# Performance work log

Hardware: AMD Instinct MI355X
Metric: run time of the kernel (lower is better)

Reference implementation:

```python
import jax, jax.numpy as jnp
import numpy as np

D_MODEL = 1024
NUM_HEADS = 16
HEAD_DIM = D_MODEL // NUM_HEADS


def setup_inputs() -> dict:
    key = jax.random.key(0)
    ks = jax.random.split(key, 9)
    B, S, D = 4, 2048, D_MODEL
    scale = 1.0 / np.sqrt(D)
    x = jax.random.normal(ks[0], (B, S, D), dtype=jnp.float32)
    wq = jax.random.normal(ks[1], (D, D), dtype=jnp.float32) * scale
    wk = jax.random.normal(ks[2], (D, D), dtype=jnp.float32) * scale
    wv = jax.random.normal(ks[3], (D, D), dtype=jnp.float32) * scale
    wo = jax.random.normal(ks[4], (D, D), dtype=jnp.float32) * scale
    bq = jax.random.normal(ks[5], (D,), dtype=jnp.float32) * 0.02
    bk = jax.random.normal(ks[6], (D,), dtype=jnp.float32) * 0.02
    bv = jax.random.normal(ks[7], (D,), dtype=jnp.float32) * 0.02
    bo = jax.random.normal(ks[8], (D,), dtype=jnp.float32) * 0.02
    return {"x": x, "wq": wq, "bq": bq, "wk": wk, "bk": bk,
            "wv": wv, "bv": bv, "wo": wo, "bo": bo}


def _split_heads(t):  # [B,S,D] -> [B,H,S,Dh]
    B, S, _ = t.shape
    return t.reshape(B, S, NUM_HEADS, HEAD_DIM).transpose(0, 2, 1, 3)


def reference(x, wq, bq, wk, bk, wv, bv, wo, bo):
    B, S, D = x.shape
    q = _split_heads(x @ wq + bq)  # [B,H,S,Dh]
    k = _split_heads(x @ wk + bk)
    v = _split_heads(x @ wv + bv)
    scores = jnp.einsum("bhqd,bhkd->bhqk", q, k) / jnp.sqrt(
        jnp.asarray(HEAD_DIM, dtype=x.dtype))
    causal = jnp.tril(jnp.ones((S, S), dtype=bool))  # [S,S]
    scores = jnp.where(causal, scores, jnp.finfo(scores.dtype).min)
    attn = jax.nn.softmax(scores, axis=-1)
    ctx = jnp.einsum("bhqk,bhkd->bhqd", attn, v)  # [B,H,S,Dh]
    ctx = ctx.transpose(0, 2, 1, 3).reshape(B, S, D)
    return ctx @ wo + bo
```

## Files before the change

### kernel.cpp

```cpp
#include <hip/hip_runtime.h>
#include <hip/hip_bf16.h>
#include <stdint.h>

#define DMODEL 1024
#define NH 16
#define DH 64
#define BATCH 4
#define SEQ 2048

#if __has_builtin(__builtin_amdgcn_exp2f)
#define EXP2F(x) __builtin_amdgcn_exp2f(x)
#else
#define EXP2F(x) exp2f(x)
#endif

typedef __attribute__((ext_vector_type(8))) short short8;
typedef __attribute__((ext_vector_type(4))) float f32x4;
typedef __attribute__((ext_vector_type(4))) ushort ushort4v;

__device__ __forceinline__ ushort f2bf(float f) {
    union { float f; unsigned u; } v; v.f = f;
    unsigned r = v.u + 0x7fffu + ((v.u >> 16) & 1u);
    return (ushort)(r >> 16);
}

__global__ __launch_bounds__(256) void convert_bf16(const float* __restrict__ src,
                                                    ushort* __restrict__ dst) {
    const size_t i = ((size_t)blockIdx.x * 256 + threadIdx.x) * 8;
    float4 a = *(const float4*)(src + i);
    float4 b = *(const float4*)(src + i + 4);
    short8 r;
    r[0] = (short)f2bf(a.x); r[1] = (short)f2bf(a.y);
    r[2] = (short)f2bf(a.z); r[3] = (short)f2bf(a.w);
    r[4] = (short)f2bf(b.x); r[5] = (short)f2bf(b.y);
    r[6] = (short)f2bf(b.z); r[7] = (short)f2bf(b.w);
    *(short8*)(dst + i) = r;
}

__global__ __launch_bounds__(256) void transpose_cvt_w4(
    const float* __restrict__ s0, const float* __restrict__ s1,
    const float* __restrict__ s2, const float* __restrict__ s3,
    ushort* __restrict__ d0, ushort* __restrict__ d1,
    ushort* __restrict__ d2, ushort* __restrict__ d3) {
    __shared__ ushort tile[64][65];
    const int z = blockIdx.z;
    const float* src = (z == 0) ? s0 : (z == 1) ? s1 : (z == 2) ? s2 : s3;
    ushort* dst = (z == 0) ? d0 : (z == 1) ? d1 : (z == 2) ? d2 : d3;
    const int bx = blockIdx.x * 64;
    const int by = blockIdx.y * 64;
    const int tx = threadIdx.x & 63, ty = threadIdx.x >> 6;
    #pragma unroll
    for (int i = 0; i < 64; i += 4)
        tile[ty + i][tx] = f2bf(src[(size_t)(by + ty + i) * DMODEL + bx + tx]);
    __syncthreads();
    #pragma unroll
    for (int i = 0; i < 64; i += 4)
        dst[(size_t)(bx + ty + i) * DMODEL + by + tx] = tile[tx][ty + i];
}

template <int MODE>
__global__ __launch_bounds__(256) void gemm_bt(
    const ushort* __restrict__ A, const ushort* __restrict__ Bt,
    const float* __restrict__ b0, const float* __restrict__ b1,
    const float* __restrict__ b2,
    void* __restrict__ o0v, void* __restrict__ o1v, void* __restrict__ o2v) {
    __shared__ __align__(16) ushort smem[8192];
    const int lane = threadIdx.x & 63;
    const int wv   = threadIdx.x >> 6;
    const int mBase = blockIdx.y * 128;
    const int nBase = blockIdx.x * 128;
    const int wm = (wv >> 1) * 64;
    const int wn = (wv & 1) * 64;

    f32x4 acc[4][4];
    #pragma unroll
    for (int i = 0; i < 4; ++i)
        #pragma unroll
        for (int j = 0; j < 4; ++j) acc[i][j] = (f32x4){0.f, 0.f, 0.f, 0.f};

    const int lrow = lane >> 2;
    const int lcol = (lane & 3) * 8;
    const int frow = lane & 15;
    const int fcol = (lane >> 4) * 8;

    for (int k0 = 0; k0 < DMODEL; k0 += 32) {
        #pragma unroll
        for (int i = 0; i < 2; ++i) {
            const int c = wv * 2 + i;
            const ushort* ga = A + (size_t)(mBase + c * 16 + lrow) * DMODEL + k0 + lcol;
            __builtin_amdgcn_global_load_lds(
                (const __attribute__((address_space(1))) void*)ga,
                (__attribute__((address_space(3))) void*)&smem[c * 512], 16, 0, 0);
            const ushort* gb = Bt + (size_t)(nBase + c * 16 + lrow) * DMODEL + k0 + lcol;
            __builtin_amdgcn_global_load_lds(
                (const __attribute__((address_space(1))) void*)gb,
                (__attribute__((address_space(3))) void*)&smem[4096 + c * 512], 16, 0, 0);
        }
        __syncthreads();
        short8 af[4], bfr[4];
        #pragma unroll
        for (int t = 0; t < 4; ++t)
            af[t] = *(const short8*)&smem[(wm + t * 16 + frow) * 32 + fcol];
        #pragma unroll
        for (int t = 0; t < 4; ++t)
            bfr[t] = *(const short8*)&smem[4096 + (wn + t * 16 + frow) * 32 + fcol];
        #pragma unroll
        for (int i = 0; i < 4; ++i)
            #pragma unroll
            for (int j = 0; j < 4; ++j)
                acc[i][j] = __builtin_amdgcn_mfma_f32_16x16x32_bf16(af[i], bfr[j],
                                                                   acc[i][j], 0, 0, 0);
        __syncthreads();
    }

    const int orow = (lane >> 4) * 4;
    const int ocol = lane & 15;

    if (MODE == 1) {
        #pragma unroll
        for (int i = 0; i < 4; ++i)
            #pragma unroll
            for (int j = 0; j < 4; ++j)
                #pragma unroll
                for (int r = 0; r < 4; ++r) {
                    const int m = mBase + wm + i * 16 + orow + r;
                    const int n = nBase + wn + j * 16 + ocol;
                    ((float*)o0v)[(size_t)m * DMODEL + n] = acc[i][j][r] + b0[n];
                }
        return;
    }

    ushort* sw = &smem[wv * 2048];
    const int mat = nBase >> 10;
    const int nb0 = (nBase & 1023) + wn;
    const int hb  = nb0 >> 6;
    const float* bp = (mat == 0) ? b0 : ((mat == 1) ? b1 : b2);
    float bj[4];
    #pragma unroll
    for (int j = 0; j < 4; ++j) bj[j] = bp[nb0 + j * 16 + ocol];
    const int bbq = (mBase + wm) >> 11;
    const int s0w = (mBase + wm) & 2047;
    const float qscale = (mat == 0) ? 0.1803368801f : 1.0f;

    if (mat < 2) {
        ushort* obase = (ushort*)((mat == 0) ? o0v : o1v) +
                        ((size_t)(bbq * NH + hb) * SEQ + s0w) * DH;
        const int row = lane >> 2, cc = lane & 3;
        #pragma unroll
        for (int i = 0; i < 4; ++i) {
            #pragma unroll
            for (int j = 0; j < 4; ++j)
                #pragma unroll
                for (int r = 0; r < 4; ++r)
                    sw[(orow + r) * 72 + j * 16 + ocol] =
                        f2bf((acc[i][j][r] + bj[j]) * qscale);
            asm volatile("s_waitcnt lgkmcnt(0)" ::: "memory");
            #pragma unroll
            for (int p = 0; p < 2; ++p) {
                short8 v8 = *(const short8*)&sw[row * 72 + cc * 8 + p * 32];
                *(short8*)&obase[(size_t)(i * 16 + row) * DH + cc * 8 + p * 32] = v8;
            }
            asm volatile("s_waitcnt lgkmcnt(0)" ::: "memory");
        }
    } else {
        ushort* op = (ushort*)o2v;
        const int rowd = lane >> 2, sc = lane & 3;
        #pragma unroll
        for (int j = 0; j < 4; ++j) {
            #pragma unroll
            for (int i = 0; i < 4; ++i)
                #pragma unroll
                for (int r = 0; r < 4; ++r)
                    sw[ocol * 72 + i * 16 + orow + r] = f2bf(acc[i][j][r] + bj[j]);
            asm volatile("s_waitcnt lgkmcnt(0)" ::: "memory");
            ushort* vbase = op + ((size_t)(bbq * NH + hb) * DH + j * 16 + rowd) * SEQ + s0w;
            #pragma unroll
            for (int p = 0; p < 2; ++p) {
                short8 v8 = *(const short8*)&sw[rowd * 72 + sc * 8 + p * 32];
                *(short8*)&vbase[sc * 8 + p * 32] = v8;
            }
            asm volatile("s_waitcnt lgkmcnt(0)" ::: "memory");
        }
    }
}

#define PSTR 72
__global__ __launch_bounds__(256, 4) void flash_attn(
    const ushort* __restrict__ Q, const ushort* __restrict__ K,
    const ushort* __restrict__ Vt, ushort* __restrict__ ctx) {
    __shared__ __align__(16) ushort Ks[4096];
    __shared__ __align__(16) ushort Vs[4096];
    __shared__ __align__(16) ushort plds[4][16 * PSTR];
    const int lane = threadIdx.x & 63;
    const int wv   = threadIdx.x >> 6;
    const int bh   = blockIdx.x & 63;
    const int Jp   = blockIdx.x >> 6;
    const int bb = bh >> 4, h = bh & 15;

    const ushort* Qb = Q + (size_t)bh * SEQ * DH;
    const ushort* Kb = K + (size_t)bh * SEQ * DH;
    const ushort* Vb = Vt + (size_t)bh * DH * SEQ;

    const int frow = lane & 15;
    const int fq   = lane >> 4;
    const int r7s  = lane >> 3;
    const int csw  = (lane & 7) ^ r7s;

    short8 ones;
    #pragma unroll
    for (int i = 0; i < 8; ++i) ones[i] = (short)0x3F80;

    #pragma unroll 1
    for (int half = 0; half < 2; ++half) {
        const int Je = half ? (31 - Jp) : Jp;
        const int q0 = Je * 64 + wv * 16;
        const int qmax = q0 + 15;

        short8 qf[2];
        #pragma unroll
        for (int ks = 0; ks < 2; ++ks)
            qf[ks] = *(const short8*)&Qb[(size_t)(q0 + frow) * DH + ks * 32 + fq * 8];

        f32x4 o[4], lacc;
        #pragma unroll
        for (int t = 0; t < 4; ++t) o[t] = (f32x4){0.f, 0.f, 0.f, 0.f};
        lacc = (f32x4){0.f, 0.f, 0.f, 0.f};

        #pragma unroll 1
        for (int it = 0; it <= Je; ++it) {
            const int k0 = it * 64;
            __syncthreads();
            #pragma unroll
            for (int i = 0; i < 2; ++i) {
                const int c = wv * 2 + i;
                const ushort* gk = Kb + (size_t)(k0 + c * 8 + r7s) * DH + csw * 8;
                __builtin_amdgcn_global_load_lds(
                    (const __attribute__((address_space(1))) void*)gk,
                    (__attribute__((address_space(3))) void*)&Ks[c * 512], 16, 0, 0);
                const ushort* gv = Vb + (size_t)(c * 8 + r7s) * SEQ + k0 + csw * 8;
                __builtin_amdgcn_global_load_lds(
                    (const __attribute__((address_space(1))) void*)gv,
                    (__attribute__((address_space(3))) void*)&Vs[c * 512], 16, 0, 0);
            }
            __syncthreads();

            if (it < Je) {
                f32x4 sacc[4];
                #pragma unroll
                for (int nt = 0; nt < 4; ++nt) sacc[nt] = (f32x4){0.f, 0.f, 0.f, 0.f};
                #pragma unroll
                for (int nt = 0; nt < 4; ++nt) {
                    const int row = nt * 16 + frow, r7 = row & 7;
                    #pragma unroll
                    for (int ks = 0; ks < 2; ++ks) {
                        short8 kf = *(const short8*)
                            &Ks[(row >> 3) * 512 + r7 * 64 + (((ks * 4 + fq) ^ r7) * 8)];
                        sacc[nt] = __builtin_amdgcn_mfma_f32_16x16x32_bf16(kf, qf[ks],
                                                                          sacc[nt], 0, 0, 0);
                    }
                }
                #pragma unroll
                for (int nt = 0; nt < 4; ++nt) {
                    float p0 = EXP2F(sacc[nt][0]);
                    float p1 = EXP2F(sacc[nt][1]);
                    float p2 = EXP2F(sacc[nt][2]);
                    float p3 = EXP2F(sacc[nt][3]);
                    uint2 dw;
                    dw.x = __builtin_amdgcn_perm(__float_as_uint(p1), __float_as_uint(p0),
                                                 0x07060302u);
                    dw.y = __builtin_amdgcn_perm(__float_as_uint(p3), __float_as_uint(p2),
                                                 0x07060302u);
                    *(uint2*)&plds[wv][frow * PSTR + nt * 16 + fq * 4] = dw;
                }
                asm volatile("s_waitcnt lgkmcnt(0)" ::: "memory");
                #pragma unroll
                for (int kc = 0; kc < 2; ++kc) {
                    short8 pf = *(const short8*)&plds[wv][frow * PSTR + kc * 32 + fq * 8];
                    lacc = __builtin_amdgcn_mfma_f32_16x16x32_bf16(ones, pf, lacc, 0, 0, 0);
                    #pragma unroll
                    for (int t = 0; t < 4; ++t) {
                        const int row = t * 16 + frow, r7 = row & 7;
                        short8 vf = *(const short8*)
                            &Vs[(row >> 3) * 512 + r7 * 64 + (((kc * 4 + fq) ^ r7) * 8)];
                        o[t] = __builtin_amdgcn_mfma_f32_16x16x32_bf16(vf, pf, o[t], 0, 0, 0);
                    }
                }
            } else {
                const int qrow = q0 + frow;
                f32x4 sacc[4];
                #pragma unroll
                for (int nt = 0; nt < 4; ++nt) sacc[nt] = (f32x4){0.f, 0.f, 0.f, 0.f};
                #pragma unroll
                for (int nt = 0; nt < 4; ++nt)
                    if (k0 + nt * 16 <= qmax) {
                        const int row = nt * 16 + frow, r7 = row & 7;
                        #pragma unroll
                        for (int ks = 0; ks < 2; ++ks) {
                            short8 kf = *(const short8*)
                                &Ks[(row >> 3) * 512 + r7 * 64 + (((ks * 4 + fq) ^ r7) * 8)];
                            sacc[nt] = __builtin_amdgcn_mfma_f32_16x16x32_bf16(kf, qf[ks],
                                                                              sacc[nt], 0, 0, 0);
                        }
                    }
                #pragma unroll
                for (int nt = 0; nt < 4; ++nt) {
                    uint2 dw; dw.x = 0u; dw.y = 0u;
                    if (k0 + nt * 16 <= qmax) {
                        float pp[4];
                        #pragma unroll
                        for (int r = 0; r < 4; ++r) {
                            const float e = EXP2F(sacc[nt][r]);
                            pp[r] = (k0 + nt * 16 + fq * 4 + r <= qrow) ? e : 0.f;
                        }
                        dw.x = __builtin_amdgcn_perm(__float_as_uint(pp[1]),
                                                     __float_as_uint(pp[0]), 0x07060302u);
                        dw.y = __builtin_amdgcn_perm(__float_as_uint(pp[3]),
                                                     __float_as_uint(pp[2]), 0x07060302u);
                    }
                    *(uint2*)&plds[wv][frow * PSTR + nt * 16 + fq * 4] = dw;
                }
                asm volatile("s_waitcnt lgkmcnt(0)" ::: "memory");
                #pragma unroll
                for (int kc = 0; kc < 2; ++kc) {
                    if (k0 + kc * 32 <= qmax) {
                        short8 pf = *(const short8*)&plds[wv][frow * PSTR + kc * 32 + fq * 8];
                        lacc = __builtin_amdgcn_mfma_f32_16x16x32_bf16(ones, pf, lacc, 0, 0, 0);
                        #pragma unroll
                        for (int t = 0; t < 4; ++t) {
                            const int row = t * 16 + frow, r7 = row & 7;
                            short8 vf = *(const short8*)
                                &Vs[(row >> 3) * 512 + r7 * 64 + (((kc * 4 + fq) ^ r7) * 8)];
                            o[t] = __builtin_amdgcn_mfma_f32_16x16x32_bf16(vf, pf, o[t], 0, 0, 0);
                        }
                    }
                }
            }
        }
        const float inv = 1.0f / lacc[0];
        const int qrow = q0 + frow;
        ushort* cp = ctx + (size_t)(bb * SEQ + qrow) * DMODEL + h * DH;
        #pragma unroll
        for (int t = 0; t < 4; ++t) {
            ushort4v ov;
            #pragma unroll
            for (int r = 0; r < 4; ++r) ov[r] = f2bf(o[t][r] * inv);
            *(ushort4v*)&cp[t * 16 + fq * 4] = ov;
        }
    }
}

extern "C" void kernel_launch(void* const* d_in, const int* in_sizes, int n_in,
                              void* d_out, int out_size, void* d_ws, size_t ws_size,
                              hipStream_t stream) {
    const float* x  = (const float*)d_in[0];
    const float* wq = (const float*)d_in[1];
    const float* bq = (const float*)d_in[2];
    const float* wk = (const float*)d_in[3];
    const float* bk = (const float*)d_in[4];
    const float* wvp = (const float*)d_in[5];
    const float* bv = (const float*)d_in[6];
    const float* wo = (const float*)d_in[7];
    const float* bo = (const float*)d_in[8];
    float* out = (float*)d_out;
    ushort* ws = (ushort*)d_ws;

    const size_t QSZ = (size_t)BATCH * NH * SEQ * DH;
    ushort* xbf   = ws;
    ushort* qws   = ws + QSZ;
    ushort* kws   = ws + 2 * QSZ;
    ushort* vtws  = ws + 3 * QSZ;
    ushort* ctxws = ws + 4 * QSZ;
    ushort* wtqkv = ws + 5 * QSZ;
    ushort* wto   = wtqkv + 3 * (size_t)DMODEL * DMODEL;

    dim3 tb(256);
    convert_bf16<<<dim3(4096), tb, 0, stream>>>(x, xbf);
    transpose_cvt_w4<<<dim3(16, 16, 4), tb, 0, stream>>>(
        wq, wk, wvp, wo,
        wtqkv, wtqkv + (size_t)DMODEL * DMODEL, wtqkv + 2 * (size_t)DMODEL * DMODEL, wto);

    gemm_bt<0><<<dim3(24, 64), tb, 0, stream>>>(xbf, wtqkv, bq, bk, bv,
                                                qws, kws, vtws);
    flash_attn<<<dim3(1024), tb, 0, stream>>>(qws, kws, vtws, ctxws);
    gemm_bt<1><<<dim3(8, 64), tb, 0, stream>>>(ctxws, wto, bo, nullptr, nullptr,
                                               out, nullptr, nullptr);
}
```

Measured before the change: 259.6 us.

## Double-buffer K/V in flash attention, fuse prep kernels, swizzle GEMM tiles per XCD

Flash attention now double-buffers the K and V tiles in LDS, issuing the next tile's global-to-LDS loads before computing the current one, with one barrier per iteration instead of two. This is meant to hide load latency. The diagonal and off-diagonal paths are merged into one loop body, and the P staging buffer is shrunk to half the width. The x conversion and weight transposes are fused into a single prep launch, and GEMM blocks are remapped so neighbouring M tiles land on the same XCD for L2 reuse. Doubling the K/V buffers raises LDS use per block, which could lower occupancy.

```diff
diff --git a/kernel.cpp b/kernel.cpp
--- a/kernel.cpp
+++ b/kernel.cpp
@@ -24,30 +24,38 @@
     return (ushort)(r >> 16);
 }
 
-__global__ __launch_bounds__(256) void convert_bf16(const float* __restrict__ src,
-                                                    ushort* __restrict__ dst) {
-    const size_t i = ((size_t)blockIdx.x * 256 + threadIdx.x) * 8;
-    float4 a = *(const float4*)(src + i);
-    float4 b = *(const float4*)(src + i + 4);
-    short8 r;
-    r[0] = (short)f2bf(a.x); r[1] = (short)f2bf(a.y);
-    r[2] = (short)f2bf(a.z); r[3] = (short)f2bf(a.w);
-    r[4] = (short)f2bf(b.x); r[5] = (short)f2bf(b.y);
-    r[6] = (short)f2bf(b.z); r[7] = (short)f2bf(b.w);
-    *(short8*)(dst + i) = r;
-}
-
-__global__ __launch_bounds__(256) void transpose_cvt_w4(
-    const float* __restrict__ s0, const float* __restrict__ s1,
-    const float* __restrict__ s2, const float* __restrict__ s3,
-    ushort* __restrict__ d0, ushort* __restrict__ d1,
-    ushort* __restrict__ d2, ushort* __restrict__ d3) {
+#define GLL(gp, lp) __builtin_amdgcn_global_load_lds( \
+    (const __attribute__((address_space(1))) void*)(gp), \
+    (__attribute__((address_space(3))) void*)(lp), 16, 0, 0)
+
+__global__ __launch_bounds__(256) void prep(
+    const float* __restrict__ x,
+    const float* __restrict__ wq, const float* __restrict__ wk,
+    const float* __restrict__ wv, const float* __restrict__ wo,
+    ushort* __restrict__ xbf,
+    ushort* __restrict__ dq, ushort* __restrict__ dk,
+    ushort* __restrict__ dv, ushort* __restrict__ dwo) {
+    const int z = blockIdx.z;
+    if (z == 4) {
+        size_t base = (size_t)(blockIdx.y * 16 + blockIdx.x) * 32768 +
+                      (size_t)threadIdx.x * 8;
+        #pragma unroll 1
+        for (int t = 0; t < 16; ++t, base += 2048) {
+            float4 a = *(const float4*)(x + base);
+            float4 c = *(const float4*)(x + base + 4);
+            short8 r;
+            r[0] = (short)f2bf(a.x); r[1] = (short)f2bf(a.y);
+            r[2] = (short)f2bf(a.z); r[3] = (short)f2bf(a.w);
+            r[4] = (short)f2bf(c.x); r[5] = (short)f2bf(c.y);
+            r[6] = (short)f2bf(c.z); r[7] = (short)f2bf(c.w);
+            *(short8*)(xbf + base) = r;
+        }
+        return;
+    }
     __shared__ ushort tile[64][65];
-    const int z = blockIdx.z;
-    const float* src = (z == 0) ? s0 : (z == 1) ? s1 : (z == 2) ? s2 : s3;
-    ushort* dst = (z == 0) ? d0 : (z == 1) ? d1 : (z == 2) ? d2 : d3;
-    const int bx = blockIdx.x * 64;
-    const int by = blockIdx.y * 64;
+    const float* src = (z == 0) ? wq : (z == 1) ? wk : (z == 2) ? wv : wo;
+    ushort* dst = (z == 0) ? dq : (z == 1) ? dk : (z == 2) ? dv : dwo;
+    const int bx = blockIdx.x * 64, by = blockIdx.y * 64;
     const int tx = threadIdx.x & 63, ty = threadIdx.x >> 6;
     #pragma unroll
     for (int i = 0; i < 64; i += 4)
@@ -67,8 +75,12 @@
     __shared__ __align__(16) ushort smem[8192];
     const int lane = threadIdx.x & 63;
     const int wv   = threadIdx.x >> 6;
-    const int mBase = blockIdx.y * 128;
-    const int nBase = blockIdx.x * 128;
+    constexpr int NTILES = (MODE == 0) ? 24 : 8;
+    const int L   = blockIdx.y * NTILES + blockIdx.x;
+    const int xcd = L & 7;
+    const int idx = L >> 3;
+    const int mBase = (xcd * 8 + idx / NTILES) * 128;
+    const int nBase = (idx % NTILES) * 128;
     const int wm = (wv >> 1) * 64;
     const int wn = (wv & 1) * 64;
 
@@ -87,14 +99,9 @@
         #pragma unroll
         for (int i = 0; i < 2; ++i) {
             const int c = wv * 2 + i;
-            const ushort* ga = A + (size_t)(mBase + c * 16 + lrow) * DMODEL + k0 + lcol;
-            __builtin_amdgcn_global_load_lds(
-                (const __attribute__((address_space(1))) void*)ga,
-                (__attribute__((address_space(3))) void*)&smem[c * 512], 16, 0, 0);
-            const ushort* gb = Bt + (size_t)(nBase + c * 16 + lrow) * DMODEL + k0 + lcol;
-            __builtin_amdgcn_global_load_lds(
-                (const __attribute__((address_space(1))) void*)gb,
-                (__attribute__((address_space(3))) void*)&smem[4096 + c * 512], 16, 0, 0);
+            GLL(A + (size_t)(mBase + c * 16 + lrow) * DMODEL + k0 + lcol, &smem[c * 512]);
+            GLL(Bt + (size_t)(nBase + c * 16 + lrow) * DMODEL + k0 + lcol,
+                &smem[4096 + c * 512]);
         }
         __syncthreads();
         short8 af[4], bfr[4];
@@ -184,13 +191,13 @@
     }
 }
 
-#define PSTR 72
+#define PSTR2 40
 __global__ __launch_bounds__(256, 4) void flash_attn(
     const ushort* __restrict__ Q, const ushort* __restrict__ K,
     const ushort* __restrict__ Vt, ushort* __restrict__ ctx) {
-    __shared__ __align__(16) ushort Ks[4096];
-    __shared__ __align__(16) ushort Vs[4096];
-    __shared__ __align__(16) ushort plds[4][16 * PSTR];
+    __shared__ __align__(16) ushort Ks[2][4096];
+    __shared__ __align__(16) ushort Vs[2][4096];
+    __shared__ __align__(16) ushort plds[4][16 * PSTR2];
     const int lane = threadIdx.x & 63;
     const int wv   = threadIdx.x >> 6;
     const int bh   = blockIdx.x & 63;
@@ -215,6 +222,7 @@
         const int Je = half ? (31 - Jp) : Jp;
         const int q0 = Je * 64 + wv * 16;
         const int qmax = q0 + 15;
+        const int qrow = q0 + frow;
 
         short8 qf[2];
         #pragma unroll
@@ -225,119 +233,88 @@
         #pragma unroll
         for (int t = 0; t < 4; ++t) o[t] = (f32x4){0.f, 0.f, 0.f, 0.f};
         lacc = (f32x4){0.f, 0.f, 0.f, 0.f};
+
+        #pragma unroll
+        for (int i = 0; i < 2; ++i) {
+            const int c = wv * 2 + i;
+            GLL(Kb + (size_t)(c * 8 + r7s) * DH + csw * 8, &Ks[0][c * 512]);
+            GLL(Vb + (size_t)(c * 8 + r7s) * SEQ + csw * 8, &Vs[0][c * 512]);
+        }
+        __syncthreads();
 
         #pragma unroll 1
         for (int it = 0; it <= Je; ++it) {
             const int k0 = it * 64;
-            __syncthreads();
-            #pragma unroll
-            for (int i = 0; i < 2; ++i) {
-                const int c = wv * 2 + i;
-                const ushort* gk = Kb + (size_t)(k0 + c * 8 + r7s) * DH + csw * 8;
-                __builtin_amdgcn_global_load_lds(
-                    (const __attribute__((address_space(1))) void*)gk,
-                    (__attribute__((address_space(3))) void*)&Ks[c * 512], 16, 0, 0);
-                const ushort* gv = Vb + (size_t)(c * 8 + r7s) * SEQ + k0 + csw * 8;
-                __builtin_amdgcn_global_load_lds(
-                    (const __attribute__((address_space(1))) void*)gv,
-                    (__attribute__((address_space(3))) void*)&Vs[c * 512], 16, 0, 0);
-            }
-            __syncthreads();
-
+            const int cur = it & 1;
             if (it < Je) {
-                f32x4 sacc[4];
                 #pragma unroll
-                for (int nt = 0; nt < 4; ++nt) sacc[nt] = (f32x4){0.f, 0.f, 0.f, 0.f};
-                #pragma unroll
-                for (int nt = 0; nt < 4; ++nt) {
+                for (int i = 0; i < 2; ++i) {
+                    const int c = wv * 2 + i;
+                    GLL(Kb + (size_t)(k0 + 64 + c * 8 + r7s) * DH + csw * 8,
+                        &Ks[cur ^ 1][c * 512]);
+                    GLL(Vb + (size_t)(c * 8 + r7s) * SEQ + k0 + 64 + csw * 8,
+                        &Vs[cur ^ 1][c * 512]);
+                }
+            }
+            const ushort* KsC = Ks[cur];
+            const ushort* VsC = Vs[cur];
+            const bool diag = (it == Je);
+
+            f32x4 sacc[4];
+            #pragma unroll
+            for (int nt = 0; nt < 4; ++nt) sacc[nt] = (f32x4){0.f, 0.f, 0.f, 0.f};
+            #pragma unroll
+            for (int nt = 0; nt < 4; ++nt) {
+                if (!diag || (k0 + nt * 16 <= qmax)) {
                     const int row = nt * 16 + frow, r7 = row & 7;
                     #pragma unroll
                     for (int ks = 0; ks < 2; ++ks) {
                         short8 kf = *(const short8*)
-                            &Ks[(row >> 3) * 512 + r7 * 64 + (((ks * 4 + fq) ^ r7) * 8)];
+                            &KsC[(row >> 3) * 512 + r7 * 64 + (((ks * 4 + fq) ^ r7) * 8)];
                         sacc[nt] = __builtin_amdgcn_mfma_f32_16x16x32_bf16(kf, qf[ks],
                                                                           sacc[nt], 0, 0, 0);
                     }
                 }
-                #pragma unroll
-                for (int nt = 0; nt < 4; ++nt) {
-                    float p0 = EXP2F(sacc[nt][0]);
-                    float p1 = EXP2F(sacc[nt][1]);
-                    float p2 = EXP2F(sacc[nt][2]);
-                    float p3 = EXP2F(sacc[nt][3]);
-                    uint2 dw;
-                    dw.x = __builtin_amdgcn_perm(__float_as_uint(p1), __float_as_uint(p0),
-                                                 0x07060302u);
-                    dw.y = __builtin_amdgcn_perm(__float_as_uint(p3), __float_as_uint(p2),
-                                                 0x07060302u);
-                    *(uint2*)&plds[wv][frow * PSTR + nt * 16 + fq * 4] = dw;
-                }
-                asm volatile("s_waitcnt lgkmcnt(0)" ::: "memory");
-                #pragma unroll
-                for (int kc = 0; kc < 2; ++kc) {
-                    short8 pf = *(const short8*)&plds[wv][frow * PSTR + kc * 32 + fq * 8];
+            }
+            #pragma unroll
+            for (int kc = 0; kc < 2; ++kc) {
+                if (!diag || (k0 + kc * 32 <= qmax)) {
+                    #pragma unroll
+                    for (int ntl = 0; ntl < 2; ++ntl) {
+                        const int nt = kc * 2 + ntl;
+                        uint2 dw; dw.x = 0u; dw.y = 0u;
+                        if (!diag || (k0 + nt * 16 <= qmax)) {
+                            float pp[4];
+                            #pragma unroll
+                            for (int r = 0; r < 4; ++r) {
+                                const float e = EXP2F(sacc[nt][r]);
+                                pp[r] = (!diag || (k0 + nt * 16 + fq * 4 + r <= qrow))
+                                            ? e : 0.f;
+                            }
+                            dw.x = __builtin_amdgcn_perm(__float_as_uint(pp[1]),
+                                                         __float_as_uint(pp[0]),
+                                                         0x07060302u);
+                            dw.y = __builtin_amdgcn_perm(__float_as_uint(pp[3]),
+                                                         __float_as_uint(pp[2]),
+                                                         0x07060302u);
+                        }
+                        *(uint2*)&plds[wv][frow * PSTR2 + ntl * 16 + fq * 4] = dw;
+                    }
+                    asm volatile("s_waitcnt lgkmcnt(0)" ::: "memory");
+                    short8 pf = *(const short8*)&plds[wv][frow * PSTR2 + fq * 8];
                     lacc = __builtin_amdgcn_mfma_f32_16x16x32_bf16(ones, pf, lacc, 0, 0, 0);
                     #pragma unroll
                     for (int t = 0; t < 4; ++t) {
                         const int row = t * 16 + frow, r7 = row & 7;
                         short8 vf = *(const short8*)
-                            &Vs[(row >> 3) * 512 + r7 * 64 + (((kc * 4 + fq) ^ r7) * 8)];
+                            &VsC[(row >> 3) * 512 + r7 * 64 + (((kc * 4 + fq) ^ r7) * 8)];
                         o[t] = __builtin_amdgcn_mfma_f32_16x16x32_bf16(vf, pf, o[t], 0, 0, 0);
                     }
                 }
-            } else {
-                const int qrow = q0 + frow;
-                f32x4 sacc[4];
-                #pragma unroll
-                for (int nt = 0; nt < 4; ++nt) sacc[nt] = (f32x4){0.f, 0.f, 0.f, 0.f};
-                #pragma unroll
-                for (int nt = 0; nt < 4; ++nt)
-                    if (k0 + nt * 16 <= qmax) {
-                        const int row = nt * 16 + frow, r7 = row & 7;
-                        #pragma unroll
-                        for (int ks = 0; ks < 2; ++ks) {
-                            short8 kf = *(const short8*)
-                                &Ks[(row >> 3) * 512 + r7 * 64 + (((ks * 4 + fq) ^ r7) * 8)];
-                            sacc[nt] = __builtin_amdgcn_mfma_f32_16x16x32_bf16(kf, qf[ks],
-                                                                              sacc[nt], 0, 0, 0);
-                        }
-                    }
-                #pragma unroll
-                for (int nt = 0; nt < 4; ++nt) {
-                    uint2 dw; dw.x = 0u; dw.y = 0u;
-                    if (k0 + nt * 16 <= qmax) {
-                        float pp[4];
-                        #pragma unroll
-                        for (int r = 0; r < 4; ++r) {
-                            const float e = EXP2F(sacc[nt][r]);
-                            pp[r] = (k0 + nt * 16 + fq * 4 + r <= qrow) ? e : 0.f;
-                        }
-                        dw.x = __builtin_amdgcn_perm(__float_as_uint(pp[1]),
-                                                     __float_as_uint(pp[0]), 0x07060302u);
-                        dw.y = __builtin_amdgcn_perm(__float_as_uint(pp[3]),
-                                                     __float_as_uint(pp[2]), 0x07060302u);
-                    }
-                    *(uint2*)&plds[wv][frow * PSTR + nt * 16 + fq * 4] = dw;
-                }
-                asm volatile("s_waitcnt lgkmcnt(0)" ::: "memory");
-                #pragma unroll
-                for (int kc = 0; kc < 2; ++kc) {
-                    if (k0 + kc * 32 <= qmax) {
-                        short8 pf = *(const short8*)&plds[wv][frow * PSTR + kc * 32 + fq * 8];
-                        lacc = __builtin_amdgcn_mfma_f32_16x16x32_bf16(ones, pf, lacc, 0, 0, 0);
-                        #pragma unroll
-                        for (int t = 0; t < 4; ++t) {
-                            const int row = t * 16 + frow, r7 = row & 7;
-                            short8 vf = *(const short8*)
-                                &Vs[(row >> 3) * 512 + r7 * 64 + (((kc * 4 + fq) ^ r7) * 8)];
-                            o[t] = __builtin_amdgcn_mfma_f32_16x16x32_bf16(vf, pf, o[t], 0, 0, 0);
-                        }
-                    }
-                }
-            }
+            }
+            __syncthreads();
         }
         const float inv = 1.0f / lacc[0];
-        const int qrow = q0 + frow;
         ushort* cp = ctx + (size_t)(bb * SEQ + qrow) * DMODEL + h * DH;
         #pragma unroll
         for (int t = 0; t < 4; ++t) {
@@ -374,10 +351,10 @@
     ushort* wto   = wtqkv + 3 * (size_t)DMODEL * DMODEL;
 
     dim3 tb(256);
-    convert_bf16<<<dim3(4096), tb, 0, stream>>>(x, xbf);
-    transpose_cvt_w4<<<dim3(16, 16, 4), tb, 0, stream>>>(
-        wq, wk, wvp, wo,
-        wtqkv, wtqkv + (size_t)DMODEL * DMODEL, wtqkv + 2 * (size_t)DMODEL * DMODEL, wto);
+    prep<<<dim3(16, 16, 5), tb, 0, stream>>>(
+        x, wq, wk, wvp, wo, xbf,
+        wtqkv, wtqkv + (size_t)DMODEL * DMODEL,
+        wtqkv + 2 * (size_t)DMODEL * DMODEL, wto);
 
     gemm_bt<0><<<dim3(24, 64), tb, 0, stream>>>(xbf, wtqkv, bq, bk, bv,
                                                 qws, kws, vtws);
```

Result: slower. 276.3 us (+6.4%).
